# Kernel tuning notes

Hardware: AMD Instinct MI355X
Metric: run time of the kernel (lower is better)

Reference implementation:

```python
import jax, jax.numpy as jnp
import numpy as np

B = 8192          # num_agents
IN_LEN = 20       # obs_len
PRED_LEN = 30     # output_len
H = 128           # h_dim
E = 64            # embedding_dim
D = 2             # data_dim
F_IN = IN_LEN * D # 40, ln1/spatial_embedding input features
LN_EPS = 1e-5


def setup_inputs() -> dict:
    key = jax.random.key(0)
    ks = jax.random.split(key, 8)
    def rn(i, shape, scale):
        return (jax.random.normal(ks[i], shape, jnp.float32) * scale).astype(jnp.float32)
    return dict(
        traj_abs=rn(0, (IN_LEN, B, D), 1.0),
        traj_rel=rn(1, (IN_LEN, B, D), 1.0),
        h0=rn(2, (1, B, H), 0.1),
        c0=rn(3, (1, B, H), 0.1),
        ln1_w=jnp.ones((F_IN,), jnp.float32),
        ln1_b=jnp.zeros((F_IN,), jnp.float32),
        emb_W=rn(4, (E, F_IN), 0.1),
        emb_b=jnp.zeros((E,), jnp.float32),
        W_ih=rn(5, (4 * H, E), 0.05),
        W_hh=rn(6, (4 * H, H), 0.05),
        b_ih=jnp.zeros((4 * H,), jnp.float32),
        b_hh=jnp.zeros((4 * H,), jnp.float32),
        ln2_w=jnp.ones((H,), jnp.float32),
        ln2_b=jnp.zeros((H,), jnp.float32),
        pos_W=rn(7, (D, H), 0.1),
        pos_b=jnp.zeros((D,), jnp.float32),
    )


def _layernorm(x, w, b):
    m = jnp.mean(x, axis=-1, keepdims=True)
    v = jnp.var(x, axis=-1, keepdims=True)
    return (x - m) * jax.lax.rsqrt(v + LN_EPS) * w + b


def reference(traj_abs, traj_rel, h0, c0, ln1_w, ln1_b, emb_W, emb_b,
              W_ih, W_hh, b_ih, b_hh, ln2_w, ln2_b, pos_W, pos_b):
    b = traj_rel.shape[1]
    h, c = h0[0], c0[0]  # num_layers=1 -> squeeze layer dim

    def step(carry, _):
        h, c, rel = carry
        # ln1 + spatial embedding + leaky_relu on raw C-order reshape (b, 40)
        x = _layernorm(rel.reshape(b, -1), ln1_w, ln1_b)
        x = jax.nn.leaky_relu(x @ emb_W.T + emb_b, negative_slope=0.01)
        # single LSTM step, torch gate order i, f, g, o
        gates = x @ W_ih.T + b_ih + h @ W_hh.T + b_hh  # (b, 4H)
        i, f, g, o = jnp.split(gates, 4, axis=-1)
        c_new = jax.nn.sigmoid(f) * c + jax.nn.sigmoid(i) * jnp.tanh(g)
        h_new = jax.nn.sigmoid(o) * jnp.tanh(c_new)
        # ln2 + hidden2pos
        rel_pos = _layernorm(h_new, ln2_w, ln2_b) @ pos_W.T + pos_b  # (b, 2)
        # roll window and write new rel position into last slot
        rel_new = jnp.concatenate([rel[1:], rel_pos[None]], axis=0)
        return (h_new, c_new, rel_new), rel_pos

    _, preds = jax.lax.scan(step, (h, c, traj_rel), None, length=PRED_LEN)
    return preds  # (pred_len, b, 2)
```

## Files before the change

### kernel.cpp

```cpp
#include <hip/hip_runtime.h>
#include <hip/hip_bf16.h>
#include <stdint.h>

#define K1 1.4426950408889634f
#define K2 2.8853900817779268f

typedef float f4 __attribute__((ext_vector_type(4)));
typedef float f2 __attribute__((ext_vector_type(2)));
typedef short s8v __attribute__((ext_vector_type(8)));
typedef unsigned int u32;
typedef unsigned short u16;

#define WS_WCAT  0
#define WS_WG    196608
#define WS_TE    204800
#define WS_SE    205056
#define WS_PWLN  205312
#define WS_SPW   206336
#define WS_PBE   206344
#define WS_BC    206352
#define WS_FLAGS 208400

#define C_WIN 0
#define C_RDY 1
#define C_RED 2
#define C_SWP 3
#define C_STT 4
#define C_PRD 5
#define C_FLG 6
#define C_PW0 7

__device__ __forceinline__ u16 f2bf(float x) {
    u32 u = __builtin_bit_cast(u32, x);
    u32 r = (u + 0x7FFFu + ((u >> 16) & 1u)) >> 16;
    return (u16)r;
}
__device__ __forceinline__ float bf2f(u16 h) {
    u32 u = ((u32)h) << 16;
    return __builtin_bit_cast(float, u);
}

__device__ __forceinline__ void waitge(u32* c, u32 v) {
    while (__hip_atomic_load(c, __ATOMIC_ACQUIRE, __HIP_MEMORY_SCOPE_WORKGROUP) < v) {}
}
__device__ __forceinline__ void waitge_s(u32* c, u32 v) {
    if (__hip_atomic_load(c, __ATOMIC_ACQUIRE, __HIP_MEMORY_SCOPE_WORKGROUP) >= v) return;
    do {
        __builtin_amdgcn_s_sleep(1);
    } while (__hip_atomic_load(c, __ATOMIC_ACQUIRE, __HIP_MEMORY_SCOPE_WORKGROUP) < v);
}
__device__ __forceinline__ void arrive(u32* c) {
    if ((threadIdx.x & 63) == 0)
        __hip_atomic_fetch_add(c, 1u, __ATOMIC_RELEASE, __HIP_MEMORY_SCOPE_WORKGROUP);
}

__global__ void prep_kernel(const float* __restrict__ ln1w, const float* __restrict__ ln1b,
                            const float* __restrict__ embW, const float* __restrict__ embB,
                            const float* __restrict__ Wih, const float* __restrict__ Whh,
                            const float* __restrict__ bih, const float* __restrict__ bhh,
                            const float* __restrict__ ln2w, const float* __restrict__ ln2b,
                            const float* __restrict__ posW, const float* __restrict__ posB,
                            char* __restrict__ ws) {
    const int tid = threadIdx.x;
    const int bid = blockIdx.x;
    u16* wcat = (u16*)(ws + WS_WCAT);

    if (bid > 0) {
        int base = (bid - 1) * 3072;
#pragma unroll 4
        for (int i = 0; i < 12; ++i) {
            int idx = base + i * 256 + tid;
            int np = idx / 192, k = idx % 192;
            int w = np >> 7, r = np & 127, nt = r >> 4, c = r & 15;
            int g = nt >> 1, jt = nt & 1;
            int n0 = (g << 7) | (w << 5) | (jt << 4) | c;
            float v = (k < 64) ? Wih[n0 * 64 + k] : Whh[n0 * 128 + (k - 64)];
            wcat[idx] = f2bf(v);
        }
        return;
    }

    u16* wg   = (u16*)(ws + WS_WG);
    float* te = (float*)(ws + WS_TE);
    float* se = (float*)(ws + WS_SE);
    float* pwln = (float*)(ws + WS_PWLN);
    float* spw  = (float*)(ws + WS_SPW);
    float* pbe  = (float*)(ws + WS_PBE);
    float* bc   = (float*)(ws + WS_BC);
    int* flags  = (int*)(ws + WS_FLAGS);
    __shared__ float pp[2][4];

    for (int idx = tid; idx < 64 * 64; idx += 256) {
        int e = idx >> 6, k = idx & 63;
        float v = (k < 40) ? embW[e * 40 + k] * ln1w[k] : 0.0f;
        wg[idx] = f2bf(v);
    }
    if (tid < 64) {
        int e = tid;
        float t = embB[e], s = 0.f;
        for (int k = 0; k < 40; ++k) {
            t += embW[e * 40 + k] * ln1b[k];
            s += bf2f(f2bf(embW[e * 40 + k] * ln1w[k]));
        }
        te[e] = t; se[e] = s;
    }
    if (tid >= 64 && tid < 192) {
        int j = tid - 64;
        float a0 = posW[j] * ln2w[j],      a1 = posW[128 + j] * ln2w[j];
        float b0 = posW[j] * ln2b[j],      b1 = posW[128 + j] * ln2b[j];
        pwln[j] = a0; pwln[128 + j] = a1;
#pragma unroll
        for (int m = 1; m < 64; m <<= 1) {
            a0 += __shfl_xor(a0, m, 64); a1 += __shfl_xor(a1, m, 64);
            b0 += __shfl_xor(b0, m, 64); b1 += __shfl_xor(b1, m, 64);
        }
        if ((tid & 63) == 0) {
            int wv = (tid >> 6) - 1;
            pp[wv][0] = a0; pp[wv][1] = a1; pp[wv][2] = b0; pp[wv][3] = b1;
        }
    }
    for (int idx = tid; idx < 512; idx += 256) {
        int w = idx >> 7, r = idx & 127, nt = r >> 4, c = r & 15;
        int g = nt >> 1, jt = nt & 1;
        int n0 = (g << 7) | (w << 5) | (jt << 4) | c;
        bc[idx] = bih[n0] + bhh[n0];
    }
    flags[tid] = 0;
    __syncthreads();
    if (tid == 0) {
        spw[0] = pp[0][0] + pp[1][0];
        spw[1] = pp[0][1] + pp[1][1];
        pbe[0] = posB[0] + pp[0][2] + pp[1][2];
        pbe[1] = posB[1] + pp[0][3] + pp[1][3];
    }
}

__global__ __launch_bounds__(768, 1)
void lstm_kernel(const float* __restrict__ traj_rel,
                 const float* __restrict__ h0, const float* __restrict__ c0,
                 float* __restrict__ dout, char* __restrict__ ws) {
    __shared__ __align__(16) u16 s_whh[12 * 512 * 8];
    __shared__ __align__(16) u16 s_x[2 * 8 * 32 * 8];
    __shared__ __align__(16) u16 s_h[2 * 16 * 32 * 8];
    __shared__ __align__(16) u16 s_win[2 * 8 * 32 * 8];
    __shared__ __align__(16) u16 s_pwb[2048];
    __shared__ __align__(16) float s_red1[4][4][32];
    __shared__ __align__(16) float s_red2[4][32];
    __shared__ __align__(16) f2 s_wp[320];
    __shared__ float s_mr[2][32][2];
    __shared__ float s_self[2][64];
    __shared__ u32 s_sync[12];

    const int tid = threadIdx.x;
    const int bk = blockIdx.x;
    const int lane = tid & 63;

    const u16* wcat = (const u16*)(ws + WS_WCAT);
    const u16* wg = (const u16*)(ws + WS_WG);
    int* flags = (int*)(ws + WS_FLAGS);

    if (tid < 12) s_sync[tid] = 0;
    for (int idx = tid; idx < 12 * 512; idx += 768) {
        const u16* src = wcat + (idx & 511) * 192 + 96 + (idx >> 9) * 8;
        *(s8v*)(s_whh + idx * 8) = *(const s8v*)src;
    }
    {
        const float* pwln = (const float*)(ws + WS_PWLN);
        for (int idx = tid; idx < 2048; idx += 768) {
            int w = idx >> 9, rem = idx & 511;
            int ksub = rem >> 7, rem2 = rem & 127;
            int n = rem2 >> 3, i = rem2 & 7;
            int j = 32 * w + ksub * 8 + i;
            float v = (n == 0) ? 1.0f : (n == 1) ? pwln[j] : (n == 2) ? pwln[128 + j] : 0.0f;
            s_pwb[(((w * 4 + ksub) * 16) + n) * 8 + i] = f2bf(v);
        }
    }
    if (tid < 192) {
        int pb = tid / 96, r = tid % 96;
        int ch = 5 + r / 32, a = r & 31;
        s8v z = {0, 0, 0, 0, 0, 0, 0, 0};
        *(s8v*)(s_win + ((pb * 8 + ch) * 32 + a) * 8) = z;
    }
    if (tid < 320) {
        int p = 1280 * bk + 4 * tid;
        f4 v = *(const f4*)(traj_rel + p);
        int a = tid / 10, kq = (tid % 10) * 4;
        u32 lo = (u32)f2bf(v[0]) | ((u32)f2bf(v[1]) << 16);
        u32 hh = (u32)f2bf(v[2]) | ((u32)f2bf(v[3]) << 16);
        u32* dst = (u32*)(s_win + ((kq >> 3) * 32 + a) * 8 + (kq & 7));
        dst[0] = lo; dst[1] = hh;
        s_wp[tid] = f2{v[0] + v[1] + v[2] + v[3],
                       v[0] * v[0] + v[1] * v[1] + v[2] * v[2] + v[3] * v[3]};
    }
    if (tid < 256) {
        int a = tid & 31, q = tid >> 5;
        const float* hp = h0 + (bk * 32 + a) * 128 + q * 16;
        u16 hb[16];
#pragma unroll
        for (int u = 0; u < 16; ++u) hb[u] = f2bf(hp[u]);
#pragma unroll
        for (int half = 0; half < 2; ++half) {
            s8v v;
#pragma unroll
            for (int u = 0; u < 8; ++u) v[u] = (short)hb[half * 8 + u];
            *(s8v*)(s_h + ((2 * q + half) * 32 + a) * 8) = v;
        }
    }
    __syncthreads();
    if (tid < 32) {
        float s = 0.f, s2 = 0.f;
#pragma unroll
        for (int u = 0; u < 10; ++u) {
            f2 p = s_wp[tid * 10 + u];
            s += p[0]; s2 += p[1];
        }
        float m = s * (1.0f / 40.0f);
        float var = s2 * (1.0f / 40.0f) - m * m;
        s_mr[0][tid][0] = m;
        s_mr[0][tid][1] = __builtin_amdgcn_rsqf(var + 1e-5f);
    }
    __syncthreads();

    if (tid < 512) {
        const int w = tid >> 6;
        const int wvi = w >> 1;
        const int jt = w & 1;
        const int cx = lane & 15;
        const int hi4 = (lane >> 4) * 4;

        s8v wih[4][2], whhr[4];
#pragma unroll
        for (int g = 0; g < 4; ++g) {
            int rowp = 128 * wvi + 16 * (2 * g + jt) + cx;
#pragma unroll
            for (int kc = 0; kc < 2; ++kc)
                wih[g][kc] = *(const s8v*)(wcat + rowp * 192 + kc * 32 + (lane >> 4) * 8);
            whhr[g] = *(const s8v*)(wcat + rowp * 192 + 64 + (lane >> 4) * 8);
        }
        s8v wgf[2];
#pragma unroll
        for (int kc = 0; kc < 2; ++kc)
            wgf[kc] = *(const s8v*)(wg + (16 * wvi + cx) * 64 + kc * 32 + (lane >> 4) * 8);

        float se_l = ((const float*)(ws + WS_SE))[16 * wvi + cx];
        float te_l = ((const float*)(ws + WS_TE))[16 * wvi + cx];
        float bias[4];
#pragma unroll
        for (int g = 0; g < 4; ++g)
            bias[g] = ((const float*)(ws + WS_BC))[128 * wvi + 16 * (2 * g + jt) + cx];
        float spw0 = ((const float*)(ws + WS_SPW))[0];
        float spw1 = ((const float*)(ws + WS_SPW))[1];
        float pbe0 = ((const float*)(ws + WS_PBE))[0];
        float pbe1 = ((const float*)(ws + WS_PBE))[1];

        float creg[2][4];
#pragma unroll
        for (int mt = 0; mt < 2; ++mt)
#pragma unroll
            for (int rg = 0; rg < 4; ++rg)
                creg[mt][rg] = c0[(bk * 32 + 16 * mt + hi4 + rg) * 128 + 32 * wvi + 16 * jt + cx];

        if (jt == 1) {
            f4 accE[2];
            accE[0] = f4{0.f, 0.f, 0.f, 0.f};
            accE[1] = f4{0.f, 0.f, 0.f, 0.f};
#pragma unroll
            for (int kc = 0; kc < 2; ++kc)
#pragma unroll
                for (int mt = 0; mt < 2; ++mt) {
                    s8v a = *(const s8v*)(s_win + ((kc * 4 + (lane >> 4)) * 32 + 16 * mt + cx) * 8);
                    accE[mt] = __builtin_amdgcn_mfma_f32_16x16x32_bf16(a, wgf[kc], accE[mt], 0, 0, 0);
                }
            int e = 16 * wvi + cx;
#pragma unroll
            for (int mt = 0; mt < 2; ++mt)
#pragma unroll
                for (int rg = 0; rg < 4; ++rg) {
                    int a = 16 * mt + hi4 + rg;
                    float m = s_mr[0][a][0], r = s_mr[0][a][1];
                    float x = r * (accE[mt][rg] - m * se_l) + te_l;
                    x = fmaxf(x, 0.f) + 0.01f * fminf(x, 0.f);
                    s_x[((e >> 3) * 32 + a) * 8 + (e & 7)] = f2bf(x);
                }
        }
        arrive(&s_sync[C_RDY]);

#pragma unroll 1
        for (int t = 0; t < 30; ++t) {
            const int pc = t & 1, pn = pc ^ 1;
            waitge(&s_sync[C_RDY], (u32)(8 * (t + 1)));

            f4 acc[2][4];
#pragma unroll
            for (int mt = 0; mt < 2; ++mt)
#pragma unroll
                for (int g = 0; g < 4; ++g)
                    acc[mt][g] = f4{bias[g], bias[g], bias[g], bias[g]};
#pragma unroll
            for (int kc = 0; kc < 6; ++kc) {
                s8v a0, a1;
                if (kc < 2) {
                    a0 = *(const s8v*)(s_x + ((pc * 8 + kc * 4 + (lane >> 4)) * 32 + cx) * 8);
                    a1 = *(const s8v*)(s_x + ((pc * 8 + kc * 4 + (lane >> 4)) * 32 + 16 + cx) * 8);
                } else {
                    int ch = (kc - 2) * 4 + (lane >> 4);
                    a0 = *(const s8v*)(s_h + ((pc * 16 + ch) * 32 + cx) * 8);
                    a1 = *(const s8v*)(s_h + ((pc * 16 + ch) * 32 + 16 + cx) * 8);
                }
#pragma unroll
                for (int g = 0; g < 4; ++g) {
                    s8v b;
                    if (kc < 2) b = wih[g][kc];
                    else if (kc == 2) b = whhr[g];
                    else b = *(const s8v*)(s_whh + (((kc - 3) * 4 + (lane >> 4)) * 512 + 128 * wvi + 16 * (2 * g + jt) + cx) * 8);
                    acc[0][g] = __builtin_amdgcn_mfma_f32_16x16x32_bf16(a0, b, acc[0][g], 0, 0, 0);
                    acc[1][g] = __builtin_amdgcn_mfma_f32_16x16x32_bf16(a1, b, acc[1][g], 0, 0, 0);
                }
            }

            {
                int kk = 32 * wvi + 16 * jt + cx;
                int ch = pn * 16 + (kk >> 3);
#pragma unroll
                for (int mt = 0; mt < 2; ++mt)
#pragma unroll
                    for (int rg = 0; rg < 4; ++rg) {
                        float iv = acc[mt][0][rg];
                        float fv = acc[mt][1][rg];
                        float gv = acc[mt][2][rg];
                        float ov = acc[mt][3][rg];
                        float si = __builtin_amdgcn_rcpf(1.f + __builtin_amdgcn_exp2f(-K1 * iv));
                        float sf = __builtin_amdgcn_rcpf(1.f + __builtin_amdgcn_exp2f(-K1 * fv));
                        float so = __builtin_amdgcn_rcpf(1.f + __builtin_amdgcn_exp2f(-K1 * ov));
                        float tg = 1.f - 2.f * __builtin_amdgcn_rcpf(1.f + __builtin_amdgcn_exp2f(K2 * gv));
                        float cn = sf * creg[mt][rg] + si * tg;
                        creg[mt][rg] = cn;
                        float tc = 1.f - 2.f * __builtin_amdgcn_rcpf(1.f + __builtin_amdgcn_exp2f(K2 * cn));
                        float hn = so * tc;
                        int a = 16 * mt + hi4 + rg;
                        s_h[(ch * 32 + a) * 8 + (cx & 7)] = f2bf(hn);
                    }
            }
            arrive(&s_sync[C_PW0 + wvi]);

            if (jt == 0) {
                waitge(&s_sync[C_PW0 + wvi], (u32)(2 * (t + 1)));
                f4 d1[2], d2[2];
                d1[0] = f4{0.f, 0.f, 0.f, 0.f}; d1[1] = f4{0.f, 0.f, 0.f, 0.f};
                d2[0] = f4{0.f, 0.f, 0.f, 0.f}; d2[1] = f4{0.f, 0.f, 0.f, 0.f};
                s8v bfrag = *(const s8v*)(s_pwb + ((wvi * 4 + (lane >> 4)) * 16 + cx) * 8);
#pragma unroll
                for (int mt = 0; mt < 2; ++mt) {
                    s8v hf = *(const s8v*)(s_h + ((pn * 16 + 4 * wvi + (lane >> 4)) * 32 + 16 * mt + cx) * 8);
                    d1[mt] = __builtin_amdgcn_mfma_f32_16x16x32_bf16(hf, bfrag, d1[mt], 0, 0, 0);
                    d2[mt] = __builtin_amdgcn_mfma_f32_16x16x32_bf16(hf, hf, d2[mt], 0, 0, 0);
                }
#pragma unroll
                for (int mt = 0; mt < 2; ++mt) {
                    if (cx < 3) {
#pragma unroll
                        for (int rg = 0; rg < 4; ++rg)
                            s_red1[wvi][cx][mt * 16 + hi4 + rg] = d1[mt][rg];
                    }
                    if ((lane >> 4) == (cx >> 2))
                        s_red2[wvi][mt * 16 + cx] = d2[mt][cx & 3];
                }
                arrive(&s_sync[C_RED]);

                if (w == 0) {
                    waitge(&s_sync[C_RED], (u32)(4 * (t + 1)));
                    int a = lane & 31, d = lane >> 5;
                    float S0 = 0.f, S1 = 0.f, P = 0.f;
#pragma unroll
                    for (int v = 0; v < 4; ++v) {
                        S0 += s_red1[v][0][a];
                        P  += s_red1[v][1 + d][a];
                        S1 += s_red2[v][a];
                    }
                    float m = S0 * (1.f / 128.f);
                    float var = S1 * (1.f / 128.f) - m * m;
                    float r = __builtin_amdgcn_rsqf(var + 1e-5f);
                    float sp = (d == 0) ? spw0 : spw1;
                    float pb = (d == 0) ? pbe0 : pbe1;
                    float val = r * (P - m * sp) + pb;
                    s_self[t & 1][2 * a + d] = val;
                    if (tid == 0)
                        __hip_atomic_store(&s_sync[C_PRD], (u32)(t + 1), __ATOMIC_RELEASE, __HIP_MEMORY_SCOPE_WORKGROUP);
                }
            } else {
                if (t < 29) {
                    waitge(&s_sync[C_WIN], (u32)(t + 1));
                    waitge(&s_sync[C_STT], (u32)(t + 1));
                    f4 accE[2];
                    accE[0] = f4{0.f, 0.f, 0.f, 0.f};
                    accE[1] = f4{0.f, 0.f, 0.f, 0.f};
#pragma unroll
                    for (int kc = 0; kc < 2; ++kc)
#pragma unroll
                        for (int mt = 0; mt < 2; ++mt) {
                            s8v a = *(const s8v*)(s_win + ((pn * 8 + kc * 4 + (lane >> 4)) * 32 + 16 * mt + cx) * 8);
                            accE[mt] = __builtin_amdgcn_mfma_f32_16x16x32_bf16(a, wgf[kc], accE[mt], 0, 0, 0);
                        }
                    int e = 16 * wvi + cx;
#pragma unroll
                    for (int mt = 0; mt < 2; ++mt)
#pragma unroll
                        for (int rg = 0; rg < 4; ++rg) {
                            int a = 16 * mt + hi4 + rg;
                            float m = s_mr[pn][a][0], r = s_mr[pn][a][1];
                            float x = r * (accE[mt][rg] - m * se_l) + te_l;
                            x = fmaxf(x, 0.f) + 0.01f * fminf(x, 0.f);
                            s_x[((pn * 8 + (e >> 3)) * 32 + a) * 8 + (e & 7)] = f2bf(x);
                        }
                }
            }
            arrive(&s_sync[C_RDY]);
        }
    } else {
        const int gt = tid - 512;

        auto stage_one = [&](int ci, int s, int pb) {
            int p = 16384 * s + 1280 * bk + 4 * ci;
            float v0, v1, v2, v3;
            if (p < 327680) {
                f4 vv = *(const f4*)(traj_rel + p);
                v0 = vv[0]; v1 = vv[1]; v2 = vv[2]; v3 = vv[3];
            } else if (bk == 255 && ci >= 304) {
                waitge_s(&s_sync[C_PRD], (u32)s);
                int o = 4 * ci - 1216;
                const float* sf = &s_self[(s - 1) & 1][0];
                v0 = sf[o]; v1 = sf[o + 1]; v2 = sf[o + 2]; v3 = sf[o + 3];
            } else {
                waitge_s(&s_sync[C_FLG], (u32)s);
                int q = p - 327680;
                f4 vv = *(const f4*)(dout + q);
                v0 = vv[0]; v1 = vv[1]; v2 = vv[2]; v3 = vv[3];
            }
            int a = ci / 10, kq = (ci % 10) * 4;
            u32 lo = (u32)f2bf(v0) | ((u32)f2bf(v1) << 16);
            u32 hh = (u32)f2bf(v2) | ((u32)f2bf(v3) << 16);
            u32* dst = (u32*)(s_win + ((pb * 8 + (kq >> 3)) * 32 + a) * 8 + (kq & 7));
            dst[0] = lo; dst[1] = hh;
            s_wp[ci] = f2{v0 + v1 + v2 + v3, v0 * v0 + v1 * v1 + v2 * v2 + v3 * v3};
        };

#pragma unroll 1
        for (int u = 0; u < 29; ++u) {
            const int pb = (u + 1) & 1;
            waitge_s(&s_sync[C_STT], (u32)u);
            waitge_s(&s_sync[C_RDY], (u32)(8 * u));

            if (gt < 64) {
                int W0n = 16384 * (u + 1) + 1280 * bk;
                int Wend = W0n + 1280;
                if (Wend > 327680) {
                    int q0 = (W0n > 327680) ? (W0n - 327680) : 0;
                    int g = (q0 >> 6) + gt;
                    int gend = (Wend - 327681) >> 6;
                    if (g <= gend) {
                        int s = g >> 8, P = g & 255;
                        if (!(bk == 255 && P == 255)) {
                            while (__hip_atomic_load(&flags[P], __ATOMIC_RELAXED, __HIP_MEMORY_SCOPE_AGENT) <= s)
                                __builtin_amdgcn_s_sleep(2);
                        }
                    }
                }
                if (gt == 0)
                    __hip_atomic_store(&s_sync[C_FLG], (u32)(u + 1), __ATOMIC_RELEASE, __HIP_MEMORY_SCOPE_WORKGROUP);
            }

            stage_one(gt, u + 1, pb);
            if (gt < 64) stage_one(gt + 256, u + 1, pb);

            arrive(&s_sync[C_SWP]);

            if ((gt >> 6) == 1) {
                waitge_s(&s_sync[C_PRD], (u32)(u + 1));
                float val = s_self[u & 1][gt & 63];
                __hip_atomic_store(dout + u * 16384 + bk * 64 + (gt & 63), val,
                                   __ATOMIC_RELAXED, __HIP_MEMORY_SCOPE_AGENT);
                asm volatile("s_waitcnt vmcnt(0)" ::: "memory");
                if (gt == 64)
                    __hip_atomic_store(&flags[bk], u + 1, __ATOMIC_RELAXED, __HIP_MEMORY_SCOPE_AGENT);
            }

            if (gt < 64) {
                waitge_s(&s_sync[C_SWP], (u32)(4 * (u + 1)));
                if (gt == 0)
                    __hip_atomic_store(&s_sync[C_WIN], (u32)(u + 1), __ATOMIC_RELEASE, __HIP_MEMORY_SCOPE_WORKGROUP);
                if (gt < 32) {
                    float s = 0.f, s2 = 0.f;
#pragma unroll
                    for (int u2 = 0; u2 < 10; ++u2) {
                        f2 pp = s_wp[gt * 10 + u2];
                        s += pp[0]; s2 += pp[1];
                    }
                    float m = s * (1.0f / 40.0f);
                    float var = s2 * (1.0f / 40.0f) - m * m;
                    s_mr[pb][gt][0] = m;
                    s_mr[pb][gt][1] = __builtin_amdgcn_rsqf(var + 1e-5f);
                }
                if (gt == 0)
                    __hip_atomic_store(&s_sync[C_STT], (u32)(u + 1), __ATOMIC_RELEASE, __HIP_MEMORY_SCOPE_WORKGROUP);
            }
        }

        if ((gt >> 6) == 1) {
            waitge_s(&s_sync[C_PRD], 30u);
            float val = s_self[1][gt & 63];
            __hip_atomic_store(dout + 29 * 16384 + bk * 64 + (gt & 63), val,
                               __ATOMIC_RELAXED, __HIP_MEMORY_SCOPE_AGENT);
        }
    }
}

extern "C" void kernel_launch(void* const* d_in, const int* in_sizes, int n_in,
                              void* d_out, int out_size, void* d_ws, size_t ws_size,
                              hipStream_t stream) {
    (void)in_sizes; (void)n_in; (void)out_size; (void)ws_size;
    const float* traj_rel = (const float*)d_in[1];
    const float* h0 = (const float*)d_in[2];
    const float* c0 = (const float*)d_in[3];
    const float* ln1w = (const float*)d_in[4];
    const float* ln1b = (const float*)d_in[5];
    const float* embW = (const float*)d_in[6];
    const float* embB = (const float*)d_in[7];
    const float* Wih = (const float*)d_in[8];
    const float* Whh = (const float*)d_in[9];
    const float* bih = (const float*)d_in[10];
    const float* bhh = (const float*)d_in[11];
    const float* ln2w = (const float*)d_in[12];
    const float* ln2b = (const float*)d_in[13];
    const float* posW = (const float*)d_in[14];
    const float* posB = (const float*)d_in[15];
    char* ws = (char*)d_ws;

    hipLaunchKernelGGL(prep_kernel, dim3(33), dim3(256), 0, stream,
                       ln1w, ln1b, embW, embB, Wih, Whh, bih, bhh, ln2w, ln2b, posW, posB, ws);
    hipLaunchKernelGGL(lstm_kernel, dim3(256), dim3(768), 0, stream,
                       traj_rel, h0, c0, (float*)d_out, ws);
}
```

Baseline: 149.7 us.

## Replace atomic counters with per-wave flag slots and spread LN2 reduction across all waves

Swaps the shared atomic fetch-add counters for per-wave monotonic flag slots (publish by store, wait by polling all slots), which removes LDS atomic contention. The LN2/hidden2pos partial MFMA is now done by all eight waves on half-width chunks, not only the jt==0 waves after a pairwise wait. The reduction buffers are double-buffered by step parity so the final reduce by wave 0 can trail the next step. The risk is more LDS polling traffic, and the correctness of the new ordering depends on the parity buffers and the monotonic slot values.

```diff
diff --git a/kernel.cpp b/kernel.cpp
--- a/kernel.cpp
+++ b/kernel.cpp
@@ -22,13 +22,9 @@
 #define WS_FLAGS 208400
 
 #define C_WIN 0
-#define C_RDY 1
-#define C_RED 2
-#define C_SWP 3
-#define C_STT 4
-#define C_PRD 5
-#define C_FLG 6
-#define C_PW0 7
+#define C_STT 1
+#define C_PRD 2
+#define C_FLG 3
 
 __device__ __forceinline__ u16 f2bf(float x) {
     u32 u = __builtin_bit_cast(u32, x);
@@ -49,9 +45,29 @@
         __builtin_amdgcn_s_sleep(1);
     } while (__hip_atomic_load(c, __ATOMIC_ACQUIRE, __HIP_MEMORY_SCOPE_WORKGROUP) < v);
 }
-__device__ __forceinline__ void arrive(u32* c) {
-    if ((threadIdx.x & 63) == 0)
-        __hip_atomic_fetch_add(c, 1u, __ATOMIC_RELEASE, __HIP_MEMORY_SCOPE_WORKGROUP);
+template <int N>
+__device__ __forceinline__ void wait_slots(volatile u32* s, u32 v) {
+    for (;;) {
+        bool ok = true;
+#pragma unroll
+        for (int i = 0; i < N; ++i) ok &= (s[i] >= v);
+        if (ok) break;
+    }
+    asm volatile("s_waitcnt lgkmcnt(0)" ::: "memory");
+}
+template <int N>
+__device__ __forceinline__ void wait_slots_s(volatile u32* s, u32 v) {
+    for (;;) {
+        bool ok = true;
+#pragma unroll
+        for (int i = 0; i < N; ++i) ok &= (s[i] >= v);
+        if (ok) break;
+        __builtin_amdgcn_s_sleep(1);
+    }
+    asm volatile("s_waitcnt lgkmcnt(0)" ::: "memory");
+}
+__device__ __forceinline__ void pub(u32* c, u32 v) {
+    __hip_atomic_store(c, v, __ATOMIC_RELEASE, __HIP_MEMORY_SCOPE_WORKGROUP);
 }
 
 __global__ void prep_kernel(const float* __restrict__ ln1w, const float* __restrict__ ln1b,
@@ -144,12 +160,15 @@
     __shared__ __align__(16) u16 s_h[2 * 16 * 32 * 8];
     __shared__ __align__(16) u16 s_win[2 * 8 * 32 * 8];
     __shared__ __align__(16) u16 s_pwb[2048];
-    __shared__ __align__(16) float s_red1[4][4][32];
-    __shared__ __align__(16) float s_red2[4][32];
+    __shared__ __align__(16) float s_red1[2][8][3][32];
+    __shared__ __align__(16) float s_red2[2][8][32];
     __shared__ __align__(16) f2 s_wp[320];
     __shared__ float s_mr[2][32][2];
     __shared__ float s_self[2][64];
-    __shared__ u32 s_sync[12];
+    __shared__ u32 s_rdy[8];
+    __shared__ u32 s_reds[8];
+    __shared__ u32 s_swp[4];
+    __shared__ u32 s_sync[4];
 
     const int tid = threadIdx.x;
     const int bk = blockIdx.x;
@@ -159,7 +178,9 @@
     const u16* wg = (const u16*)(ws + WS_WG);
     int* flags = (int*)(ws + WS_FLAGS);
 
-    if (tid < 12) s_sync[tid] = 0;
+    if (tid < 8) { s_rdy[tid] = 0; s_reds[tid] = 0; }
+    if (tid >= 8 && tid < 12) s_swp[tid - 8] = 0;
+    if (tid >= 12 && tid < 16) s_sync[tid - 12] = 0;
     for (int idx = tid; idx < 12 * 512; idx += 768) {
         const u16* src = wcat + (idx & 511) * 192 + 96 + (idx >> 9) * 8;
         *(s8v*)(s_whh + idx * 8) = *(const s8v*)src;
@@ -167,12 +188,12 @@
     {
         const float* pwln = (const float*)(ws + WS_PWLN);
         for (int idx = tid; idx < 2048; idx += 768) {
-            int w = idx >> 9, rem = idx & 511;
-            int ksub = rem >> 7, rem2 = rem & 127;
+            int w = idx >> 8, rem = idx & 255;
+            int kb = rem >> 7, rem2 = rem & 127;
             int n = rem2 >> 3, i = rem2 & 7;
-            int j = 32 * w + ksub * 8 + i;
-            float v = (n == 0) ? 1.0f : (n == 1) ? pwln[j] : (n == 2) ? pwln[128 + j] : 0.0f;
-            s_pwb[(((w * 4 + ksub) * 16) + n) * 8 + i] = f2bf(v);
+            int col = 32 * (w >> 1) + 16 * (w & 1) + kb * 8 + i;
+            float v = (n == 0) ? 1.0f : (n == 1) ? pwln[col] : (n == 2) ? pwln[128 + col] : 0.0f;
+            s_pwb[(((w * 2 + kb) * 16) + n) * 8 + i] = f2bf(v);
         }
     }
     if (tid < 192) {
@@ -227,6 +248,7 @@
         const int jt = w & 1;
         const int cx = lane & 15;
         const int hi4 = (lane >> 4) * 4;
+        const bool lohalf = (lane >> 4) < 2;
 
         s8v wih[4][2], whhr[4];
 #pragma unroll
@@ -241,6 +263,9 @@
 #pragma unroll
         for (int kc = 0; kc < 2; ++kc)
             wgf[kc] = *(const s8v*)(wg + (16 * wvi + cx) * 64 + kc * 32 + (lane >> 4) * 8);
+        s8v bfrag = {0, 0, 0, 0, 0, 0, 0, 0};
+        if (lohalf)
+            bfrag = *(const s8v*)(s_pwb + (((w * 2 + (lane >> 4)) * 16) + cx) * 8);
 
         float se_l = ((const float*)(ws + WS_SE))[16 * wvi + cx];
         float te_l = ((const float*)(ws + WS_TE))[16 * wvi + cx];
@@ -283,12 +308,13 @@
                     s_x[((e >> 3) * 32 + a) * 8 + (e & 7)] = f2bf(x);
                 }
         }
-        arrive(&s_sync[C_RDY]);
+        if (lane == 0) pub(&s_rdy[w], 1u);
 
 #pragma unroll 1
         for (int t = 0; t < 30; ++t) {
             const int pc = t & 1, pn = pc ^ 1;
-            waitge(&s_sync[C_RDY], (u32)(8 * (t + 1)));
+            const int sb = t & 1;
+            wait_slots<8>(s_rdy, (u32)(t + 1));
 
             f4 acc[2][4];
 #pragma unroll
@@ -341,17 +367,17 @@
                         s_h[(ch * 32 + a) * 8 + (cx & 7)] = f2bf(hn);
                     }
             }
-            arrive(&s_sync[C_PW0 + wvi]);
-
-            if (jt == 0) {
-                waitge(&s_sync[C_PW0 + wvi], (u32)(2 * (t + 1)));
+
+            {
                 f4 d1[2], d2[2];
                 d1[0] = f4{0.f, 0.f, 0.f, 0.f}; d1[1] = f4{0.f, 0.f, 0.f, 0.f};
                 d2[0] = f4{0.f, 0.f, 0.f, 0.f}; d2[1] = f4{0.f, 0.f, 0.f, 0.f};
-                s8v bfrag = *(const s8v*)(s_pwb + ((wvi * 4 + (lane >> 4)) * 16 + cx) * 8);
+                int ch0 = 4 * wvi + 2 * jt;
 #pragma unroll
                 for (int mt = 0; mt < 2; ++mt) {
-                    s8v hf = *(const s8v*)(s_h + ((pn * 16 + 4 * wvi + (lane >> 4)) * 32 + 16 * mt + cx) * 8);
+                    s8v hf = {0, 0, 0, 0, 0, 0, 0, 0};
+                    if (lohalf)
+                        hf = *(const s8v*)(s_h + ((pn * 16 + ch0 + (lane >> 4)) * 32 + 16 * mt + cx) * 8);
                     d1[mt] = __builtin_amdgcn_mfma_f32_16x16x32_bf16(hf, bfrag, d1[mt], 0, 0, 0);
                     d2[mt] = __builtin_amdgcn_mfma_f32_16x16x32_bf16(hf, hf, d2[mt], 0, 0, 0);
                 }
@@ -360,61 +386,60 @@
                     if (cx < 3) {
 #pragma unroll
                         for (int rg = 0; rg < 4; ++rg)
-                            s_red1[wvi][cx][mt * 16 + hi4 + rg] = d1[mt][rg];
+                            s_red1[sb][w][cx][mt * 16 + hi4 + rg] = d1[mt][rg];
                     }
                     if ((lane >> 4) == (cx >> 2))
-                        s_red2[wvi][mt * 16 + cx] = d2[mt][cx & 3];
-                }
-                arrive(&s_sync[C_RED]);
-
-                if (w == 0) {
-                    waitge(&s_sync[C_RED], (u32)(4 * (t + 1)));
-                    int a = lane & 31, d = lane >> 5;
-                    float S0 = 0.f, S1 = 0.f, P = 0.f;
-#pragma unroll
-                    for (int v = 0; v < 4; ++v) {
-                        S0 += s_red1[v][0][a];
-                        P  += s_red1[v][1 + d][a];
-                        S1 += s_red2[v][a];
+                        s_red2[sb][w][mt * 16 + cx] = d2[mt][cx & 3];
+                }
+                if (lane == 0) pub(&s_reds[w], (u32)(t + 1));
+            }
+
+            if (jt == 1 && t < 29) {
+                waitge(&s_sync[C_WIN], (u32)(t + 1));
+                waitge(&s_sync[C_STT], (u32)(t + 1));
+                f4 accE[2];
+                accE[0] = f4{0.f, 0.f, 0.f, 0.f};
+                accE[1] = f4{0.f, 0.f, 0.f, 0.f};
+#pragma unroll
+                for (int kc = 0; kc < 2; ++kc)
+#pragma unroll
+                    for (int mt = 0; mt < 2; ++mt) {
+                        s8v a = *(const s8v*)(s_win + ((pn * 8 + kc * 4 + (lane >> 4)) * 32 + 16 * mt + cx) * 8);
+                        accE[mt] = __builtin_amdgcn_mfma_f32_16x16x32_bf16(a, wgf[kc], accE[mt], 0, 0, 0);
                     }
-                    float m = S0 * (1.f / 128.f);
-                    float var = S1 * (1.f / 128.f) - m * m;
-                    float r = __builtin_amdgcn_rsqf(var + 1e-5f);
-                    float sp = (d == 0) ? spw0 : spw1;
-                    float pb = (d == 0) ? pbe0 : pbe1;
-                    float val = r * (P - m * sp) + pb;
-                    s_self[t & 1][2 * a + d] = val;
-                    if (tid == 0)
-                        __hip_atomic_store(&s_sync[C_PRD], (u32)(t + 1), __ATOMIC_RELEASE, __HIP_MEMORY_SCOPE_WORKGROUP);
-                }
-            } else {
-                if (t < 29) {
-                    waitge(&s_sync[C_WIN], (u32)(t + 1));
-                    waitge(&s_sync[C_STT], (u32)(t + 1));
-                    f4 accE[2];
-                    accE[0] = f4{0.f, 0.f, 0.f, 0.f};
-                    accE[1] = f4{0.f, 0.f, 0.f, 0.f};
-#pragma unroll
-                    for (int kc = 0; kc < 2; ++kc)
-#pragma unroll
-                        for (int mt = 0; mt < 2; ++mt) {
-                            s8v a = *(const s8v*)(s_win + ((pn * 8 + kc * 4 + (lane >> 4)) * 32 + 16 * mt + cx) * 8);
-                            accE[mt] = __builtin_amdgcn_mfma_f32_16x16x32_bf16(a, wgf[kc], accE[mt], 0, 0, 0);
-                        }
-                    int e = 16 * wvi + cx;
-#pragma unroll
-                    for (int mt = 0; mt < 2; ++mt)
-#pragma unroll
-                        for (int rg = 0; rg < 4; ++rg) {
-                            int a = 16 * mt + hi4 + rg;
-                            float m = s_mr[pn][a][0], r = s_mr[pn][a][1];
-                            float x = r * (accE[mt][rg] - m * se_l) + te_l;
-                            x = fmaxf(x, 0.f) + 0.01f * fminf(x, 0.f);
-                            s_x[((pn * 8 + (e >> 3)) * 32 + a) * 8 + (e & 7)] = f2bf(x);
-                        }
-                }
-            }
-            arrive(&s_sync[C_RDY]);
+                int e = 16 * wvi + cx;
+#pragma unroll
+                for (int mt = 0; mt < 2; ++mt)
+#pragma unroll
+                    for (int rg = 0; rg < 4; ++rg) {
+                        int a = 16 * mt + hi4 + rg;
+                        float m = s_mr[pn][a][0], r = s_mr[pn][a][1];
+                        float x = r * (accE[mt][rg] - m * se_l) + te_l;
+                        x = fmaxf(x, 0.f) + 0.01f * fminf(x, 0.f);
+                        s_x[((pn * 8 + (e >> 3)) * 32 + a) * 8 + (e & 7)] = f2bf(x);
+                    }
+            }
+            if (lane == 0) pub(&s_rdy[w], (u32)(t + 2));
+
+            if (w == 0) {
+                wait_slots<8>(s_reds, (u32)(t + 1));
+                int a = lane & 31, d = lane >> 5;
+                float S0 = 0.f, S1 = 0.f, P = 0.f;
+#pragma unroll
+                for (int v2 = 0; v2 < 8; ++v2) {
+                    S0 += s_red1[sb][v2][0][a];
+                    P  += s_red1[sb][v2][1 + d][a];
+                    S1 += s_red2[sb][v2][a];
+                }
+                float m = S0 * (1.f / 128.f);
+                float var = S1 * (1.f / 128.f) - m * m;
+                float r = __builtin_amdgcn_rsqf(var + 1e-5f);
+                float sp = (d == 0) ? spw0 : spw1;
+                float pb = (d == 0) ? pbe0 : pbe1;
+                float val = r * (P - m * sp) + pb;
+                s_self[t & 1][2 * a + d] = val;
+                if (tid == 0) pub(&s_sync[C_PRD], (u32)(t + 1));
+            }
         }
     } else {
         const int gt = tid - 512;
@@ -448,7 +473,7 @@
         for (int u = 0; u < 29; ++u) {
             const int pb = (u + 1) & 1;
             waitge_s(&s_sync[C_STT], (u32)u);
-            waitge_s(&s_sync[C_RDY], (u32)(8 * u));
+            wait_slots_s<8>(s_rdy, (u32)u);
 
             if (gt < 64) {
                 int W0n = 16384 * (u + 1) + 1280 * bk;
@@ -465,14 +490,13 @@
                         }
                     }
                 }
-                if (gt == 0)
-                    __hip_atomic_store(&s_sync[C_FLG], (u32)(u + 1), __ATOMIC_RELEASE, __HIP_MEMORY_SCOPE_WORKGROUP);
+                if (gt == 0) pub(&s_sync[C_FLG], (u32)(u + 1));
             }
 
             stage_one(gt, u + 1, pb);
             if (gt < 64) stage_one(gt + 256, u + 1, pb);
 
-            arrive(&s_sync[C_SWP]);
+            if ((gt & 63) == 0) pub(&s_swp[gt >> 6], (u32)(u + 1));
 
             if ((gt >> 6) == 1) {
                 waitge_s(&s_sync[C_PRD], (u32)(u + 1));
@@ -485,9 +509,8 @@
             }
 
             if (gt < 64) {
-                waitge_s(&s_sync[C_SWP], (u32)(4 * (u + 1)));
-                if (gt == 0)
-                    __hip_atomic_store(&s_sync[C_WIN], (u32)(u + 1), __ATOMIC_RELEASE, __HIP_MEMORY_SCOPE_WORKGROUP);
+                wait_slots_s<4>(s_swp, (u32)(u + 1));
+                if (gt == 0) pub(&s_sync[C_WIN], (u32)(u + 1));
                 if (gt < 32) {
                     float s = 0.f, s2 = 0.f;
 #pragma unroll
@@ -500,8 +523,7 @@
                     s_mr[pb][gt][0] = m;
                     s_mr[pb][gt][1] = __builtin_amdgcn_rsqf(var + 1e-5f);
                 }
-                if (gt == 0)
-                    __hip_atomic_store(&s_sync[C_STT], (u32)(u + 1), __ATOMIC_RELEASE, __HIP_MEMORY_SCOPE_WORKGROUP);
+                if (gt == 0) pub(&s_sync[C_STT], (u32)(u + 1));
             }
         }
 
```

After: 202.6 us. 1.35x slower.
